# Kernel tuning notes

Measured on AMD Instinct MI355X. Metric: run time of the kernel, lower is better.

## Reference

```python
import jax, jax.numpy as jnp
import numpy as np

B, T, D = 2, 2048, 2048
H, KVH = 16, 4
HD = D // H            # 128
HALF = HD // 2         # 64
EPS = 1e-6


def zc_rmsnorm(x, scale):
    # zero-centred RMSNorm: (1+scale) * x / rms(x), rms in fp32
    rms = jnp.sqrt(jnp.mean(x.astype(jnp.float32) ** 2, axis=-1, keepdims=True) + EPS)
    return ((1.0 + scale) * x / rms).astype(x.dtype)


def apply_rope(x, cos, sin):
    # x: [B, h, T, HD]; cos/sin: [T, HALF]
    t = x.shape[2]
    c = cos[:t][None, None, :, :]
    s = sin[:t][None, None, :, :]
    x1, x2 = x[..., :HALF], x[..., HALF:]
    return jnp.concatenate([x1 * c - x2 * s, x2 * c + x1 * s], axis=-1)


def setup_inputs() -> dict:
    key = jax.random.key(0)
    ks = jax.random.split(key, 8)
    std = 0.02
    res_std = 0.02 / np.sqrt(2 * 24)
    q_input = jax.random.normal(ks[0], (B, T, D), jnp.float32)
    kv_input = jax.random.normal(ks[1], (B, T, D), jnp.float32)
    mask = jnp.tril(jnp.ones((T, T), bool))[None, None, :, :]
    inv_freq = 1.0 / (10000.0 ** (jnp.arange(0, HALF, dtype=jnp.float32) / HALF))
    ang = jnp.arange(T, dtype=jnp.float32)[:, None] * inv_freq[None, :]
    cos, sin = jnp.cos(ang), jnp.sin(ang)
    Wq = jax.random.normal(ks[2], (D, D), jnp.float32) * std
    Wk = jax.random.normal(ks[3], (D, KVH * HD), jnp.float32) * std
    Wv = jax.random.normal(ks[4], (D, KVH * HD), jnp.float32) * std
    q_scale = jnp.zeros((HD,), jnp.float32)
    k_scale = jnp.zeros((HD,), jnp.float32)
    Wo = jax.random.normal(ks[5], (D, D), jnp.float32) * res_std
    return {"q_input": q_input, "kv_input": kv_input, "mask": mask,
            "cos": cos, "sin": sin, "Wq": Wq, "Wk": Wk, "Wv": Wv,
            "q_scale": q_scale, "k_scale": k_scale, "Wo": Wo}


def reference(q_input, kv_input, mask, cos, sin, Wq, Wk, Wv, q_scale, k_scale, Wo):
    b = q_input.shape[0]
    q = (q_input @ Wq).reshape(b, -1, H, HD).transpose(0, 2, 1, 3)      # [B,H,T,HD]
    k = (kv_input @ Wk).reshape(b, -1, KVH, HD).transpose(0, 2, 1, 3)   # [B,KVH,T,HD]
    v = (kv_input @ Wv).reshape(b, -1, KVH, HD).transpose(0, 2, 1, 3)
    q = zc_rmsnorm(q, q_scale)
    k = zc_rmsnorm(k, k_scale)
    rep = H // KVH
    k = jnp.repeat(k, rep, axis=1)
    v = jnp.repeat(v, rep, axis=1)
    q = apply_rope(q, cos, sin)
    k = apply_rope(k, cos, sin)
    scale = jnp.sqrt(jnp.float32(HD))
    scores = jnp.einsum('bhqd,bhkd->bhqk', q, k) / scale                # [B,H,T,T]
    scores = jnp.where(mask, scores, jnp.finfo(scores.dtype).min)
    attn = jax.nn.softmax(scores, axis=-1)
    out = jnp.einsum('bhqk,bhkd->bhqd', attn, v)
    out = out.transpose(0, 2, 1, 3).reshape(b, -1, D)
    return out @ Wo
```

## Files before the change

### kernel.cpp

```cpp
#include <hip/hip_runtime.h>

#define NB 2
#define NT 2048
#define ND 2048
#define NH 16
#define NKVH 4
#define NHD 128
#define NHALF 64
#define NREP (NH / NKVH)
#define MFIX 12.0f

typedef __bf16 bf16x8 __attribute__((ext_vector_type(8)));
typedef unsigned short u16x8 __attribute__((ext_vector_type(8)));
typedef unsigned short u16x4 __attribute__((ext_vector_type(4)));
typedef float f32x4 __attribute__((ext_vector_type(4)));

__device__ __forceinline__ unsigned short f2b(float f) {
  union { __bf16 h; unsigned short u; } v;
  v.h = (__bf16)f;
  return v.u;
}

__device__ __forceinline__ void glds16(const unsigned short* g, unsigned short* l) {
  __builtin_amdgcn_global_load_lds(
      (__attribute__((address_space(1))) unsigned int*)(unsigned long long)g,
      (__attribute__((address_space(3))) unsigned int*)(unsigned int)(unsigned long long)l,
      16, 0, 0);
}

__device__ __forceinline__ void f2bf_body(const float* __restrict__ in,
                                          unsigned short* __restrict__ out, int lb) {
  const size_t i = (size_t)(lb * 256 + threadIdx.x) * 8;
  float4 a = *(const float4*)(in + i);
  float4 b = *(const float4*)(in + i + 4);
  u16x8 r;
  r[0] = f2b(a.x); r[1] = f2b(a.y); r[2] = f2b(a.z); r[3] = f2b(a.w);
  r[4] = f2b(b.x); r[5] = f2b(b.y); r[6] = f2b(b.z); r[7] = f2b(b.w);
  *(u16x8*)(out + i) = r;
}

__device__ __forceinline__ void wtrans_body(const float* __restrict__ in,
                                            unsigned short* __restrict__ out,
                                            int K, int N, int bx, int by,
                                            float (*tile)[33]) {
  const int k0 = by * 32, n0 = bx * 32;
  const int x = threadIdx.x & 31, y8 = threadIdx.x >> 5;
#pragma unroll
  for (int j = 0; j < 4; ++j) {
    const int y = y8 + j * 8;
    tile[y][x] = in[(size_t)(k0 + y) * N + n0 + x];
  }
  __syncthreads();
#pragma unroll
  for (int j = 0; j < 4; ++j) {
    const int y = y8 + j * 8;
    out[(size_t)(n0 + y) * K + k0 + x] = f2b(tile[x][y]);
  }
}

__global__ __launch_bounds__(256) void prep_all(const float* __restrict__ q_input,
                                                unsigned short* __restrict__ Qb16,
                                                const float* __restrict__ kv_input,
                                                unsigned short* __restrict__ KVb16,
                                                const float* __restrict__ Wq,
                                                unsigned short* __restrict__ Wqt,
                                                const float* __restrict__ Wk,
                                                const float* __restrict__ Wv,
                                                unsigned short* __restrict__ WkvT,
                                                const float* __restrict__ Wo,
                                                unsigned short* __restrict__ Wot) {
  __shared__ float tile[32][33];
  const int l = blockIdx.x;
  if (l < 4096) {
    f2bf_body(q_input, Qb16, l);
  } else if (l < 8192) {
    f2bf_body(kv_input, KVb16, l - 4096);
  } else if (l < 12288) {
    const int l2 = l - 8192;
    wtrans_body(Wq, Wqt, 2048, 2048, l2 & 63, l2 >> 6, tile);
  } else if (l < 13312) {
    const int l2 = l - 12288;
    wtrans_body(Wk, WkvT, 2048, 512, l2 & 15, l2 >> 4, tile);
  } else if (l < 14336) {
    const int l2 = l - 13312;
    wtrans_body(Wv, WkvT + (size_t)512 * 2048, 2048, 512, l2 & 15, l2 >> 4, tile);
  } else {
    const int l2 = l - 14336;
    wtrans_body(Wo, Wot, 2048, 2048, l2 & 63, l2 >> 6, tile);
  }
}


__device__ __forceinline__ void gemm_mm_db(const unsigned short* __restrict__ A,
                                           const unsigned short* __restrict__ Bt,
                                           int K, int m0, int n0,
                                           unsigned short* As, unsigned short* Bs,
                                           f32x4 (&acc)[4][4]) {
  const int tid = threadIdx.x;
  const int wave = tid >> 6, lane = tid & 63;
  const int wm = wave >> 1, wn = wave & 1;
  const int quad = lane >> 4, c = lane & 15;
  const int lr = lane >> 3;
  const int gsw = ((lane & 7) ^ lr) * 8;

  const unsigned short* pa[4];
  const unsigned short* pb[4];
  unsigned short* da[4];
  unsigned short* db[4];
#pragma unroll
  for (int j = 0; j < 4; ++j) {
    const int rb = j * 32 + wave * 8;
    pa[j] = A + (size_t)(m0 + rb + lr) * K + gsw;
    pb[j] = Bt + (size_t)(n0 + rb + lr) * K + gsw;
    da[j] = As + rb * 64;
    db[j] = Bs + rb * 64;
  }

  const f32x4 zero = {0.f, 0.f, 0.f, 0.f};
#pragma unroll
  for (int sm = 0; sm < 4; ++sm)
#pragma unroll
    for (int sn = 0; sn < 4; ++sn) acc[sm][sn] = zero;

  const int nsteps = K >> 6;
  int cur = 0;
#pragma unroll
  for (int j = 0; j < 4; ++j) { glds16(pa[j], da[j]); glds16(pb[j], db[j]); }
  __syncthreads();

  for (int t = 0; t < nsteps; ++t) {
    const int nxt = (cur ^ 1) * (128 * 64);
    if (t + 1 < nsteps) {
      const int kn = (t + 1) << 6;
#pragma unroll
      for (int j = 0; j < 4; ++j) {
        glds16(pa[j] + kn, da[j] + nxt);
        glds16(pb[j] + kn, db[j] + nxt);
      }
    }
    const unsigned short* Ab = As + cur * (128 * 64);
    const unsigned short* Bb = Bs + cur * (128 * 64);
#pragma unroll
    for (int kk = 0; kk < 2; ++kk) {
      const int g = ((kk * 4 + quad) ^ (c & 7)) * 8;
      bf16x8 af[4];
#pragma unroll
      for (int sm = 0; sm < 4; ++sm)
        af[sm] = *(const bf16x8*)&Ab[(wm * 64 + sm * 16 + c) * 64 + g];
#pragma unroll
      for (int sn = 0; sn < 4; ++sn) {
        bf16x8 bfr = *(const bf16x8*)&Bb[(wn * 64 + sn * 16 + c) * 64 + g];
#pragma unroll
        for (int sm = 0; sm < 4; ++sm)
          acc[sm][sn] = __builtin_amdgcn_mfma_f32_16x16x32_bf16(af[sm], bfr, acc[sm][sn], 0, 0, 0);
      }
    }
    __syncthreads();
    cur ^= 1;
  }
}

__device__ __forceinline__ void gemm_mm_sb(const unsigned short* __restrict__ A,
                                           const unsigned short* __restrict__ Bt,
                                           int K, int m0, int n0,
                                           unsigned short* As, unsigned short* Bs,
                                           f32x4 (&acc)[4][4]) {
  const int tid = threadIdx.x;
  const int wave = tid >> 6, lane = tid & 63;
  const int wm = wave >> 1, wn = wave & 1;
  const int quad = lane >> 4, c = lane & 15;
  const int lr = lane >> 3;
  const int gsw = ((lane & 7) ^ lr) * 8;

  const unsigned short* pa[4];
  const unsigned short* pb[4];
  unsigned short* da[4];
  unsigned short* db[4];
#pragma unroll
  for (int j = 0; j < 4; ++j) {
    const int rb = j * 32 + wave * 8;
    pa[j] = A + (size_t)(m0 + rb + lr) * K + gsw;
    pb[j] = Bt + (size_t)(n0 + rb + lr) * K + gsw;
    da[j] = As + rb * 64;
    db[j] = Bs + rb * 64;
  }

  const f32x4 zero = {0.f, 0.f, 0.f, 0.f};
#pragma unroll
  for (int sm = 0; sm < 4; ++sm)
#pragma unroll
    for (int sn = 0; sn < 4; ++sn) acc[sm][sn] = zero;

  const int nsteps = K >> 6;
  for (int t = 0; t < nsteps; ++t) {
    const int kn = t << 6;
#pragma unroll
    for (int j = 0; j < 4; ++j) {
      glds16(pa[j] + kn, da[j]);
      glds16(pb[j] + kn, db[j]);
    }
    __syncthreads();
#pragma unroll
    for (int kk = 0; kk < 2; ++kk) {
      const int g = ((kk * 4 + quad) ^ (c & 7)) * 8;
      bf16x8 af[4];
#pragma unroll
      for (int sm = 0; sm < 4; ++sm)
        af[sm] = *(const bf16x8*)&As[(wm * 64 + sm * 16 + c) * 64 + g];
#pragma unroll
      for (int sn = 0; sn < 4; ++sn) {
        bf16x8 bfr = *(const bf16x8*)&Bs[(wn * 64 + sn * 16 + c) * 64 + g];
#pragma unroll
        for (int sm = 0; sm < 4; ++sm)
          acc[sm][sn] = __builtin_amdgcn_mfma_f32_16x16x32_bf16(af[sm], bfr, acc[sm][sn], 0, 0, 0);
      }
    }
    __syncthreads();
  }
}

__global__ __launch_bounds__(256) void gemm128(const unsigned short* __restrict__ A,
                                               const unsigned short* __restrict__ Bt,
                                               float* __restrict__ C,
                                               int M, int N, int K) {
  __shared__ __align__(16) unsigned char smem[65536];
  unsigned short* As = (unsigned short*)smem;
  unsigned short* Bs = (unsigned short*)(smem + 32768);
  const int gx = gridDim.x;
  const int nwg = gx * gridDim.y;
  int lin = blockIdx.y * gx + blockIdx.x;
  lin = (lin & 7) * (nwg >> 3) + (lin >> 3);
  const int m0 = (lin / gx) * 128, n0 = (lin % gx) * 128;
  f32x4 acc[4][4];
  gemm_mm_db(A, Bt, K, m0, n0, As, Bs, acc);
  const int tid = threadIdx.x;
  const int wave = tid >> 6, lane = tid & 63;
  const int wm = wave >> 1, wn = wave & 1;
  const int quad = lane >> 4, c = lane & 15;
#pragma unroll
  for (int sm = 0; sm < 4; ++sm)
#pragma unroll
    for (int sn = 0; sn < 4; ++sn) {
      const int row = m0 + wm * 64 + sm * 16 + quad * 4;
      const int col = n0 + wn * 64 + sn * 16 + c;
#pragma unroll
      for (int r = 0; r < 4; ++r)
        C[(size_t)(row + r) * N + col] = acc[sm][sn][r];
    }
}

__device__ __forceinline__ void epi_normrope(f32x4 (&acc)[4][4], float* xb,
                                             unsigned short* __restrict__ dst,
                                             const float* __restrict__ scale,
                                             const float* __restrict__ cosp,
                                             const float* __restrict__ sinp,
                                             int t0, float outscale) {
  const int tid = threadIdx.x;
  const int wave = tid >> 6, lane = tid & 63;
  const int wm = wave >> 1, wn = wave & 1;
  const int quad = lane >> 4, c = lane & 15;
#pragma unroll
  for (int p = 0; p < 2; ++p) {
#pragma unroll
    for (int ls = 0; ls < 2; ++ls) {
      const int sm = 2 * p + ls;
      const int lrow = wm * 32 + ls * 16 + quad * 4;
#pragma unroll
      for (int sn = 0; sn < 4; ++sn) {
        const int col = wn * 64 + sn * 16 + c;
#pragma unroll
        for (int r = 0; r < 4; ++r)
          xb[(lrow + r) * 128 + col] = acc[sm][sn][r];
      }
    }
    __syncthreads();
#pragma unroll
    for (int ls = 0; ls < 2; ++ls) {
      const int sm = 2 * p + ls;
#pragma unroll
      for (int r = 0; r < 4; ++r) {
        const int lrow = wm * 32 + ls * 16 + quad * 4 + r;
        const int row = wm * 64 + sm * 16 + quad * 4 + r;
        float par[4];
        float ps = 0.f;
#pragma unroll
        for (int sn = 0; sn < 4; ++sn) {
          const float own = acc[sm][sn][r];
          par[sn] = xb[lrow * 128 + ((wn ^ 1) * 64 + sn * 16 + c)];
          ps += own * own + par[sn] * par[sn];
        }
        ps += __shfl_xor(ps, 1, 64);
        ps += __shfl_xor(ps, 2, 64);
        ps += __shfl_xor(ps, 4, 64);
        ps += __shfl_xor(ps, 8, 64);
        const float inv = 1.0f / sqrtf(ps * (1.0f / NHD) + 1e-6f);
        const int t = t0 + row;
#pragma unroll
        for (int sn = 0; sn < 4; ++sn) {
          const int d = wn * 64 + sn * 16 + c;
          const int dd = sn * 16 + c;
          const float n_own = (1.0f + scale[d]) * acc[sm][sn][r] * inv;
          const float n_par = (1.0f + scale[d ^ 64]) * par[sn] * inv;
          const float cc = cosp[t * NHALF + dd], ss = sinp[t * NHALF + dd];
          const float o = (wn == 0) ? (n_own * cc - n_par * ss)
                                    : (n_own * cc + n_par * ss);
          dst[(size_t)row * NHD + d] = f2b(o * outscale);
        }
      }
    }
    __syncthreads();
  }
}

__device__ __forceinline__ void epi_vtrans(f32x4 (&acc)[4][4],
                                           unsigned short* vb,
                                           unsigned short* __restrict__ dst) {
  const int tid = threadIdx.x;
  const int wave = tid >> 6, lane = tid & 63;
  const int wm = wave >> 1, wn = wave & 1;
  const int quad = lane >> 4, c = lane & 15;
#pragma unroll
  for (int p = 0; p < 2; ++p) {
#pragma unroll
    for (int sm = 0; sm < 4; ++sm)
#pragma unroll
      for (int ls = 0; ls < 2; ++ls) {
        const int sn = 2 * p + ls;
        const int row = wm * 64 + sm * 16 + quad * 4;
        const int lcol = wn * 32 + ls * 16 + c;
        u16x4 pk;
        pk[0] = f2b(acc[sm][sn][0]); pk[1] = f2b(acc[sm][sn][1]);
        pk[2] = f2b(acc[sm][sn][2]); pk[3] = f2b(acc[sm][sn][3]);
        *(u16x4*)&vb[lcol * 136 + row] = pk;
      }
    __syncthreads();
#pragma unroll
    for (int i = 0; i < 16; ++i) {
      const int lcol = wave * 16 + i;
      const int d = (lcol >> 5) * 64 + (2 * p + ((lcol >> 4) & 1)) * 16 + (lcol & 15);
      const unsigned int v = *(const unsigned int*)&vb[lcol * 136 + lane * 2];
      *(unsigned int*)&dst[(size_t)d * NT + lane * 2] = v;
    }
    __syncthreads();
  }
}

__global__ __launch_bounds__(256) void gemm_qkv(const unsigned short* __restrict__ Aq,
                                                const unsigned short* __restrict__ Wqt,
                                                const unsigned short* __restrict__ Akv,
                                                const unsigned short* __restrict__ Wkv,
                                                unsigned short* __restrict__ Qh,
                                                unsigned short* __restrict__ Kh,
                                                unsigned short* __restrict__ Vtg,
                                                const float* __restrict__ q_scale,
                                                const float* __restrict__ k_scale,
                                                const float* __restrict__ cosp,
                                                const float* __restrict__ sinp) {
  __shared__ __align__(16) unsigned char smem[32768];
  unsigned short* As = (unsigned short*)smem;
  unsigned short* Bs = (unsigned short*)(smem + 16384);
  int lin = blockIdx.x;
  lin = (lin & 7) * 96 + (lin >> 3);
  f32x4 acc[4][4];
  if (lin < 512) {
    const int m0 = (lin >> 4) * 128, n0 = (lin & 15) * 128;
    gemm_mm_sb(Aq, Wqt, 2048, m0, n0, As, Bs, acc);
    const int b = m0 >> 11, t0 = m0 & 2047, h = n0 >> 7;
    epi_normrope(acc, (float*)smem,
                 Qh + ((size_t)(b * NH + h) * NT + t0) * NHD,
                 q_scale, cosp, sinp, t0, 0.08838834764831845f);
  } else {
    const int l2 = lin - 512;
    const int m0 = (l2 >> 3) * 128, n0 = (l2 & 7) * 128;
    gemm_mm_sb(Akv, Wkv, 2048, m0, n0, As, Bs, acc);
    const int b = m0 >> 11, t0 = m0 & 2047;
    if (n0 < 512) {
      const int g = n0 >> 7;
      epi_normrope(acc, (float*)smem,
                   Kh + ((size_t)(b * NKVH + g) * NT + t0) * NHD,
                   k_scale, cosp, sinp, t0, 1.0f);
    } else {
      const int g = (n0 - 512) >> 7;
      epi_vtrans(acc, (unsigned short*)smem,
                 Vtg + ((size_t)(b * NKVH + g) * NHD) * NT + t0);
    }
  }
}

__global__ __launch_bounds__(256, 3) void attn64(const unsigned short* __restrict__ Qh,
                                                 const unsigned short* __restrict__ Kh,
                                                 const unsigned short* __restrict__ Vtg,
                                                 unsigned short* __restrict__ O) {
  __shared__ unsigned short Kt[64 * 132];
  __shared__ unsigned short Vt[128 * 68];
  __shared__ unsigned short Pt[64 * 68];
  const int bh = blockIdx.x;
  const int b = bh / NH, h = bh % NH, g = h / NREP;
  const int y = blockIdx.y;
  const int a = y & 7, bb = y >> 3;
  const int qt = (bb == 0) ? a : (bb == 1) ? a + 8 : (bb == 2) ? 31 - a : 23 - a;
  const int tid = threadIdx.x;
  const int w = tid >> 6, lane = tid & 63;
  const int quad = lane >> 4, c = lane & 15;

  bf16x8 qf[4];
  {
    const unsigned short* qp =
        Qh + ((size_t)(b * NH + h) * NT + qt * 64 + w * 16 + c) * NHD + quad * 8;
#pragma unroll
    for (int ch = 0; ch < 4; ++ch) qf[ch] = *(const bf16x8*)(qp + ch * 32);
  }

  f32x4 acc_o[8] = {};
  float lsum[4] = {0.f, 0.f, 0.f, 0.f};
  const size_t kbase = (size_t)(b * NKVH + g) * NT * NHD;
  const size_t vbase = (size_t)(b * NKVH + g) * NHD * NT;
  const int nkt = qt + 1;

  u16x8 kreg[4], vreg[4];
#pragma unroll
  for (int j = 0; j < 4; ++j) {
    const int f = j * 256 + tid;
    kreg[j] = *(const u16x8*)&Kh[kbase + (size_t)(f >> 4) * NHD + (f & 15) * 8];
    vreg[j] = *(const u16x8*)&Vtg[vbase + (size_t)(f >> 3) * NT + (f & 7) * 8];
  }

  for (int kt = 0; kt < nkt; ++kt) {
#pragma unroll
    for (int j = 0; j < 4; ++j) {
      const int f = j * 256 + tid;
      *(u16x8*)&Kt[(f >> 4) * 132 + (f & 15) * 8] = kreg[j];
      *(u16x8*)&Vt[(f >> 3) * 68 + (f & 7) * 8] = vreg[j];
    }
    __syncthreads();

    if (kt + 1 < nkt) {
      const int k0 = (kt + 1) * 64;
#pragma unroll
      for (int j = 0; j < 4; ++j) {
        const int f = j * 256 + tid;
        kreg[j] = *(const u16x8*)&Kh[kbase + (size_t)(k0 + (f >> 4)) * NHD + (f & 15) * 8];
        vreg[j] = *(const u16x8*)&Vtg[vbase + (size_t)(f >> 3) * NT + k0 + (f & 7) * 8];
      }
    }

    f32x4 s[4] = {};
#pragma unroll
    for (int n = 0; n < 4; ++n)
#pragma unroll
      for (int ch = 0; ch < 4; ++ch) {
        bf16x8 kf = *(const bf16x8*)&Kt[(n * 16 + c) * 132 + ch * 32 + quad * 8];
        s[n] = __builtin_amdgcn_mfma_f32_16x16x32_bf16(qf[ch], kf, s[n], 0, 0, 0);
      }

    const bool dmask = (kt == qt);
#pragma unroll
    for (int r = 0; r < 4; ++r) {
      float v0 = s[0][r], v1 = s[1][r], v2 = s[2][r], v3 = s[3][r];
      const int lrow = w * 16 + quad * 4 + r;
      if (dmask) {
        if (c > lrow) v0 = -1e30f;
        if (16 + c > lrow) v1 = -1e30f;
        if (32 + c > lrow) v2 = -1e30f;
        if (48 + c > lrow) v3 = -1e30f;
      }
      const float p0 = __expf(v0 - MFIX), p1 = __expf(v1 - MFIX);
      const float p2 = __expf(v2 - MFIX), p3 = __expf(v3 - MFIX);
      lsum[r] += (p0 + p1) + (p2 + p3);
      Pt[lrow * 68 + c] = f2b(p0);
      Pt[lrow * 68 + 16 + c] = f2b(p1);
      Pt[lrow * 68 + 32 + c] = f2b(p2);
      Pt[lrow * 68 + 48 + c] = f2b(p3);
    }

#pragma unroll
    for (int kc2 = 0; kc2 < 2; ++kc2) {
      bf16x8 pf = *(const bf16x8*)&Pt[(w * 16 + c) * 68 + kc2 * 32 + quad * 8];
#pragma unroll
      for (int n2 = 0; n2 < 8; ++n2) {
        bf16x8 vf = *(const bf16x8*)&Vt[(n2 * 16 + c) * 68 + kc2 * 32 + quad * 8];
        acc_o[n2] = __builtin_amdgcn_mfma_f32_16x16x32_bf16(pf, vf, acc_o[n2], 0, 0, 0);
      }
    }
    __syncthreads();
  }

#pragma unroll
  for (int r = 0; r < 4; ++r) {
    float l = lsum[r];
    l += __shfl_xor(l, 1, 64);
    l += __shfl_xor(l, 2, 64);
    l += __shfl_xor(l, 4, 64);
    l += __shfl_xor(l, 8, 64);
    lsum[r] = l;
  }

#pragma unroll
  for (int r = 0; r < 4; ++r) {
    const float invl = 1.0f / lsum[r];
    const int qrow = qt * 64 + w * 16 + quad * 4 + r;
    unsigned short* op = O + ((size_t)(b * NT + qrow) * NH + h) * NHD + c;
#pragma unroll
    for (int n2 = 0; n2 < 8; ++n2) op[n2 * 16] = f2b(acc_o[n2][r] * invl);
  }
}

extern "C" void kernel_launch(void* const* d_in, const int* in_sizes, int n_in,
                              void* d_out, int out_size, void* d_ws, size_t ws_size,
                              hipStream_t stream) {
  (void)in_sizes; (void)n_in; (void)out_size; (void)ws_size;
  const float* q_input  = (const float*)d_in[0];
  const float* kv_input = (const float*)d_in[1];
  const float* cosp = (const float*)d_in[3];
  const float* sinp = (const float*)d_in[4];
  const float* Wq = (const float*)d_in[5];
  const float* Wk = (const float*)d_in[6];
  const float* Wv = (const float*)d_in[7];
  const float* q_scale = (const float*)d_in[8];
  const float* k_scale = (const float*)d_in[9];
  const float* Wo = (const float*)d_in[10];
  float* out = (float*)d_out;

  char* p = (char*)d_ws;
  unsigned short* Qb16  = (unsigned short*)p; p += (size_t)NB * NT * ND * 2;
  unsigned short* KVb16 = (unsigned short*)p; p += (size_t)NB * NT * ND * 2;
  unsigned short* Qh  = (unsigned short*)p; p += (size_t)NB * NH * NT * NHD * 2;
  unsigned short* Kh  = (unsigned short*)p; p += (size_t)NB * NKVH * NT * NHD * 2;
  unsigned short* Vtg = (unsigned short*)p; p += (size_t)NB * NKVH * NT * NHD * 2;
  unsigned short* Wqt  = (unsigned short*)p; p += (size_t)ND * ND * 2;
  unsigned short* WkvT = (unsigned short*)p; p += (size_t)1024 * ND * 2;
  unsigned short* Wot  = (unsigned short*)p; p += (size_t)ND * ND * 2;
  unsigned short* Ob = Qb16;

  const dim3 blk(256);
  const int M = NB * NT;

  prep_all<<<dim3(18432), blk, 0, stream>>>(q_input, Qb16, kv_input, KVb16,
                                            Wq, Wqt, Wk, Wv, WkvT, Wo, Wot);

  gemm_qkv<<<dim3(768), blk, 0, stream>>>(Qb16, Wqt, KVb16, WkvT,
                                          Qh, Kh, Vtg, q_scale, k_scale, cosp, sinp);

  attn64<<<dim3(NB * NH, 32), blk, 0, stream>>>(Qh, Kh, Vtg, Ob);

  gemm128<<<dim3(ND / 128, M / 128), blk, 0, stream>>>(Ob, Wot, out, M, ND, ND);
}
```

Baseline: 361.1 us.

## Double-buffer QKV projection GEMM with 32-wide K tiles and manual bf16 rounding

Replaces the single-buffered 64-wide K-step GEMM used in the fused QKV projection kernel with a double-buffered 32-wide K-step version. The next tile's global-to-LDS loads are issued before the MFMAs on the current tile, so loads overlap compute and one barrier per step is removed, while the 32 KB LDS budget stays the same. The fp32-to-bf16 conversion also becomes integer round-to-nearest-even bit manipulation instead of the compiler cast, which may change NaN handling. The smaller K step halves the MFMA work per barrier, so barrier overhead per step is relatively higher.

Result: no change. 356.9 us (-1.2%).

```diff
diff --git a/kernel.cpp b/kernel.cpp
--- a/kernel.cpp
+++ b/kernel.cpp
@@ -16,9 +16,9 @@
 typedef float f32x4 __attribute__((ext_vector_type(4)));
 
 __device__ __forceinline__ unsigned short f2b(float f) {
-  union { __bf16 h; unsigned short u; } v;
-  v.h = (__bf16)f;
-  return v.u;
+  union { float f; unsigned int u; } v; v.f = f;
+  unsigned int r = v.u + 0x7FFFu + ((v.u >> 16) & 1u);
+  return (unsigned short)(r >> 16);
 }
 
 __device__ __forceinline__ void glds16(const unsigned short* g, unsigned short* l) {
@@ -90,7 +90,6 @@
   }
 }
 
-
 __device__ __forceinline__ void gemm_mm_db(const unsigned short* __restrict__ A,
                                            const unsigned short* __restrict__ Bt,
                                            int K, int m0, int n0,
@@ -160,7 +159,7 @@
   }
 }
 
-__device__ __forceinline__ void gemm_mm_sb(const unsigned short* __restrict__ A,
+__device__ __forceinline__ void gemm_mm_32(const unsigned short* __restrict__ A,
                                            const unsigned short* __restrict__ Bt,
                                            int K, int m0, int n0,
                                            unsigned short* As, unsigned short* Bs,
@@ -169,20 +168,20 @@
   const int wave = tid >> 6, lane = tid & 63;
   const int wm = wave >> 1, wn = wave & 1;
   const int quad = lane >> 4, c = lane & 15;
-  const int lr = lane >> 3;
-  const int gsw = ((lane & 7) ^ lr) * 8;
-
-  const unsigned short* pa[4];
-  const unsigned short* pb[4];
-  unsigned short* da[4];
-  unsigned short* db[4];
-#pragma unroll
-  for (int j = 0; j < 4; ++j) {
-    const int rb = j * 32 + wave * 8;
+  const int lr = lane >> 2;
+  const int gsw = ((lane & 3) ^ (lr & 3)) * 8;
+
+  const unsigned short* pa[2];
+  const unsigned short* pb[2];
+  unsigned short* da[2];
+  unsigned short* db[2];
+#pragma unroll
+  for (int j = 0; j < 2; ++j) {
+    const int rb = j * 64 + wave * 16;
     pa[j] = A + (size_t)(m0 + rb + lr) * K + gsw;
     pb[j] = Bt + (size_t)(n0 + rb + lr) * K + gsw;
-    da[j] = As + rb * 64;
-    db[j] = Bs + rb * 64;
+    da[j] = As + rb * 32;
+    db[j] = Bs + rb * 32;
   }
 
   const f32x4 zero = {0.f, 0.f, 0.f, 0.f};
@@ -191,31 +190,38 @@
 #pragma unroll
     for (int sn = 0; sn < 4; ++sn) acc[sm][sn] = zero;
 
-  const int nsteps = K >> 6;
+  const int nsteps = K >> 5;
+  int cur = 0;
+#pragma unroll
+  for (int j = 0; j < 2; ++j) { glds16(pa[j], da[j]); glds16(pb[j], db[j]); }
+  __syncthreads();
+
   for (int t = 0; t < nsteps; ++t) {
-    const int kn = t << 6;
-#pragma unroll
-    for (int j = 0; j < 4; ++j) {
-      glds16(pa[j] + kn, da[j]);
-      glds16(pb[j] + kn, db[j]);
-    }
-    __syncthreads();
-#pragma unroll
-    for (int kk = 0; kk < 2; ++kk) {
-      const int g = ((kk * 4 + quad) ^ (c & 7)) * 8;
-      bf16x8 af[4];
+    const int nxt = (cur ^ 1) * (128 * 32);
+    if (t + 1 < nsteps) {
+      const int kn = (t + 1) << 5;
+#pragma unroll
+      for (int j = 0; j < 2; ++j) {
+        glds16(pa[j] + kn, da[j] + nxt);
+        glds16(pb[j] + kn, db[j] + nxt);
+      }
+    }
+    const unsigned short* Ab = As + cur * (128 * 32);
+    const unsigned short* Bb = Bs + cur * (128 * 32);
+    const int g = (quad ^ (c & 3)) * 8;
+    bf16x8 af[4];
+#pragma unroll
+    for (int sm = 0; sm < 4; ++sm)
+      af[sm] = *(const bf16x8*)&Ab[(wm * 64 + sm * 16 + c) * 32 + g];
+#pragma unroll
+    for (int sn = 0; sn < 4; ++sn) {
+      bf16x8 bfr = *(const bf16x8*)&Bb[(wn * 64 + sn * 16 + c) * 32 + g];
 #pragma unroll
       for (int sm = 0; sm < 4; ++sm)
-        af[sm] = *(const bf16x8*)&As[(wm * 64 + sm * 16 + c) * 64 + g];
-#pragma unroll
-      for (int sn = 0; sn < 4; ++sn) {
-        bf16x8 bfr = *(const bf16x8*)&Bs[(wn * 64 + sn * 16 + c) * 64 + g];
-#pragma unroll
-        for (int sm = 0; sm < 4; ++sm)
-          acc[sm][sn] = __builtin_amdgcn_mfma_f32_16x16x32_bf16(af[sm], bfr, acc[sm][sn], 0, 0, 0);
-      }
-    }
-    __syncthreads();
+        acc[sm][sn] = __builtin_amdgcn_mfma_f32_16x16x32_bf16(af[sm], bfr, acc[sm][sn], 0, 0, 0);
+    }
+    __syncthreads();
+    cur ^= 1;
   }
 }
 
@@ -364,7 +370,7 @@
   f32x4 acc[4][4];
   if (lin < 512) {
     const int m0 = (lin >> 4) * 128, n0 = (lin & 15) * 128;
-    gemm_mm_sb(Aq, Wqt, 2048, m0, n0, As, Bs, acc);
+    gemm_mm_32(Aq, Wqt, 2048, m0, n0, As, Bs, acc);
     const int b = m0 >> 11, t0 = m0 & 2047, h = n0 >> 7;
     epi_normrope(acc, (float*)smem,
                  Qh + ((size_t)(b * NH + h) * NT + t0) * NHD,
@@ -372,7 +378,7 @@
   } else {
     const int l2 = lin - 512;
     const int m0 = (l2 >> 3) * 128, n0 = (l2 & 7) * 128;
-    gemm_mm_sb(Akv, Wkv, 2048, m0, n0, As, Bs, acc);
+    gemm_mm_32(Akv, Wkv, 2048, m0, n0, As, Bs, acc);
     const int b = m0 >> 11, t0 = m0 & 2047;
     if (n0 < 512) {
       const int g = n0 >> 7;
```
